# Performance work log

Hardware: AMD Instinct MI355X
Metric: run time of the kernel (lower is better)

Reference implementation:

```python
import jax, jax.numpy as jnp
import numpy as np

K_NEIGHBORS = 16  # n_sample

# Each Conv1x1+BatchNorm (eval mode) stage is an exact per-channel affine map,
# so it is represented by a single fused (W, b) pair: y = W @ x + b.

def affine(W, b, x):
    # W: [Cout, Cin]; x: [B, Cin, N] or [B, Cin, N, K]
    if x.ndim == 3:
        return jnp.einsum('oc,bcn->bon', W, x) + b[None, :, None]
    return jnp.einsum('oc,bcnk->bonk', W, x) + b[None, :, None, None]

def knn_idx(p, k):
    # p: [B, N, 3] -> idx of k nearest neighbors (incl. self): [B, N, k]
    sq = jnp.sum(p * p, axis=-1)  # [B, N]
    d2 = sq[:, :, None] + sq[:, None, :] - 2.0 * jnp.einsum('bnc,bmc->bnm', p, p)
    _, idx = jax.lax.top_k(-d2, k)
    return idx

def group(feat, idx):
    # feat: [B, C, N], idx: [B, N, K] -> grouped[b,c,n,k] = feat[b,c,idx[b,n,k]]
    return jax.vmap(lambda f, i: f[:, i])(feat, idx)


def setup_inputs() -> dict:
    key = jax.random.key(0)
    B, C, N = 4, 128, 4096
    ks = jax.random.split(key, 22)
    def w(k, o, i):
        return (jax.random.normal(k, (o, i), jnp.float32) / np.sqrt(i)).astype(jnp.float32)
    def bv(k, o):
        return (jax.random.normal(k, (o,), jnp.float32) * 0.01).astype(jnp.float32)
    inp = {
        'input_p': jax.random.normal(ks[0], (B, 3, N), jnp.float32),
        'input_x': jax.random.normal(ks[1], (B, C, N), jnp.float32),
        'top_W': w(ks[2], C, C),   'top_b': bv(ks[3], C),
        'down_W': w(ks[4], C, C),  'down_b': bv(ks[5], C),
        'phi_W': w(ks[6], C, C),   'phi_b': bv(ks[7], C),
        'psi_W': w(ks[8], C, C),   'psi_b': bv(ks[9], C),
        'alpha_W': w(ks[10], C, C), 'alpha_b': bv(ks[11], C),
        'g1_W': w(ks[12], C, C),   'g1_b': bv(ks[13], C),
        'g2_W': w(ks[14], C, C),   'g2_b': bv(ks[15], C),
        'd1_W': w(ks[16], C, 3),   'd1_b': bv(ks[17], C),
        'd2_W': w(ks[18], C, C),   'd2_b': bv(ks[19], C),
        'a': 0, 'b': 0,
    }
    return inp


def reference(input_p, input_x, top_W, top_b, down_W, down_b, phi_W, phi_b,
              psi_W, psi_b, alpha_W, alpha_b, g1_W, g1_b, g2_W, g2_b,
              d1_W, d1_b, d2_W, d2_b, a, b):
    res = input_x
    p = jnp.transpose(input_p, (0, 2, 1))          # [B, N, 3]
    idx = knn_idx(p, K_NEIGHBORS)                  # [B, N, K]
    grouped_p = group(input_p, idx)                # [B, 3, N, K]
    x = affine(top_W, top_b, input_x)              # linear_top
    phi = affine(phi_W, phi_b, x)[:, :, :, None]   # [B, C, N, 1] (broadcast over K)
    psi = group(affine(psi_W, psi_b, x), idx)      # [B, C, N, K]
    alp = group(affine(alpha_W, alpha_b, x), idx)  # [B, C, N, K]
    rel = input_p[:, :, :, None] - grouped_p       # relative xyz [B, 3, N, K]
    pos = affine(d2_W, d2_b, jax.nn.relu(affine(d1_W, d1_b, rel)))   # delta MLP
    attn = affine(g2_W, g2_b, jax.nn.relu(affine(g1_W, g1_b, phi - psi + pos)))  # gamma MLP
    y = (jax.nn.softmax(attn, axis=-1) * (alp + pos)).sum(axis=-1)   # [B, C, N]
    y = affine(down_W, down_b, y)                  # linear_down
    return y + res
```

## Files before the change

### kernel.cpp

```cpp
#include <hip/hip_runtime.h>
#include <hip/hip_bf16.h>

#define BB 4
#define CC 128
#define NN 4096
#define KK 16
#define FLT_BIG 3.402823466e+38f

typedef __attribute__((ext_vector_type(8))) short short8v;
typedef __attribute__((ext_vector_type(4))) short short4v;
typedef __attribute__((ext_vector_type(4))) float f32x4;

__device__ __forceinline__ unsigned short f2b(float x) {
  union { float f; unsigned u; } v; v.f = x;
  unsigned r = v.u + 0x7fffu + ((v.u >> 16) & 1u);
  return (unsigned short)(r >> 16);
}
__device__ __forceinline__ float b2f(unsigned short h) {
  union { float f; unsigned u; } v; v.u = ((unsigned)h) << 16; return v.f;
}

__device__ __forceinline__ float dist4(const float4 q, const float4 c) {
  float t = __fmaf_rn(q.x, c.x, __fmaf_rn(q.y, c.y, __fmul_rn(q.z, c.z)));
  return __fmaf_rn(-2.f, t, q.w + c.w);
}

__global__ __launch_bounds__(256) void prep_kernel(const float* __restrict__ p,
                                                   float4* __restrict__ pkg) {
  int i = blockIdx.x * 256 + threadIdx.x;
  int b = i >> 12, m = i & (NN - 1);
  const float* pb = p + (size_t)b * 3 * NN;
  float x = pb[m], y = pb[NN + m], z = pb[2 * NN + m];
  pkg[i] = make_float4(x, y, z, __fmaf_rn(x, x, __fmaf_rn(y, y, __fmul_rn(z, z))));
}

__global__ __launch_bounds__(256) void wprep_kernel(
    const float* __restrict__ d2W, const float* __restrict__ g1W,
    const float* __restrict__ g2W, const float* __restrict__ topW,
    const float* __restrict__ phiW, const float* __restrict__ psiW,
    const float* __restrict__ alpW, const float* __restrict__ dnW,
    unsigned short* __restrict__ wpk) {
  int t = blockIdx.x * 256 + threadIdx.x;
  int mat = t >> 11, r = t & 2047;
  int ct = r >> 8, ks = (r >> 6) & 3, lane = r & 63;
  const float* W;
  switch (mat) {
    case 0: W = d2W; break;  case 1: W = g1W; break;
    case 2: W = g2W; break;  case 3: W = topW; break;
    case 4: W = phiW; break; case 5: W = psiW; break;
    case 6: W = alpW; break; default: W = dnW; break;
  }
  int row = ct * 16 + (lane & 15);
  int k0 = ks * 32 + (lane >> 4) * 8;
  const float* src = &W[row * 128 + k0];
  unsigned short* dh = &wpk[((size_t)(((mat * 2 + 0) * 8 + ct) * 4 + ks) * 64 + lane) * 8];
  unsigned short* dl = &wpk[((size_t)(((mat * 2 + 1) * 8 + ct) * 4 + ks) * 64 + lane) * 8];
#pragma unroll
  for (int e = 0; e < 8; ++e) {
    float v = src[e];
    unsigned short h = f2b(v);
    dh[e] = h;
    dl[e] = f2b(v - b2f(h));
  }
}

__global__ __launch_bounds__(256) void xpose_kernel(const float* __restrict__ x,
                                                    unsigned short* __restrict__ xh,
                                                    unsigned short* __restrict__ xl) {
  __shared__ float t[64][65];
  const int b = blockIdx.z, c0 = blockIdx.y * 64, n0 = blockIdx.x * 64;
  const int tn = threadIdx.x & 63, tq = threadIdx.x >> 6;
  const float* xb = x + ((size_t)b * CC + c0) * NN + n0;
#pragma unroll
  for (int i = 0; i < 16; ++i) {
    int c = tq * 16 + i;
    t[c][tn] = xb[(size_t)c * NN + tn];
  }
  __syncthreads();
#pragma unroll
  for (int i = 0; i < 16; ++i) {
    int nl = tq * 16 + i;
    float v = t[tn][nl];
    unsigned short h = f2b(v);
    size_t o = ((size_t)b * NN + n0 + nl) * CC + c0 + tn;
    xh[o] = h;
    xl[o] = f2b(v - b2f(h));
  }
}

__global__ __launch_bounds__(512, 2) void knn_kernel(const float4* __restrict__ pkg,
                                                     int* __restrict__ outidx)
{
  __shared__ float BD[8][64][17];
  __shared__ float TS[64];
  __shared__ int   CNT[64];
  __shared__ float COLd[64][20];
  __shared__ int   COLi[64][20];
  const int b = blockIdx.y;
  const int tid = threadIdx.x;
  const int lane = tid & 63;
  const int w = tid >> 6;
  const int n = blockIdx.x * 64 + lane;
  const float4* PB = pkg + (size_t)b * NN;
  const float4 qc = PB[n];
  if (tid < 64) CNT[tid] = 0;

  float bd[16];
#pragma unroll
  for (int t = 0; t < 16; ++t) bd[t] = FLT_BIG;
  const int m0 = w * 512;
#pragma unroll 4
  for (int m = m0; m < m0 + 512; ++m) {
    float4 c = PB[m];
    float d = dist4(qc, c);
#pragma unroll
    for (int t = 15; t >= 1; --t) bd[t] = __builtin_amdgcn_fmed3f(bd[t - 1], d, bd[t]);
    bd[0] = fminf(bd[0], d);
  }
#pragma unroll
  for (int t = 0; t < 16; ++t) BD[w][lane][t] = bd[t];
  __syncthreads();

  if (tid < 64) {
    const int q = tid;
    int h0 = 0, h1 = 0, h2 = 0, h3 = 0, h4 = 0, h5 = 0, h6 = 0, h7 = 0;
    float mv = FLT_BIG;
#pragma unroll 1
    for (int r = 0; r < 16; ++r) {
      float v0 = BD[0][q][h0], v1 = BD[1][q][h1], v2 = BD[2][q][h2], v3 = BD[3][q][h3];
      float v4 = BD[4][q][h4], v5 = BD[5][q][h5], v6 = BD[6][q][h6], v7 = BD[7][q][h7];
      mv = v0; int mw = 0;
      if (v1 < mv) { mv = v1; mw = 1; }
      if (v2 < mv) { mv = v2; mw = 2; }
      if (v3 < mv) { mv = v3; mw = 3; }
      if (v4 < mv) { mv = v4; mw = 4; }
      if (v5 < mv) { mv = v5; mw = 5; }
      if (v6 < mv) { mv = v6; mw = 6; }
      if (v7 < mv) { mv = v7; mw = 7; }
      h0 += (mw == 0); h1 += (mw == 1); h2 += (mw == 2); h3 += (mw == 3);
      h4 += (mw == 4); h5 += (mw == 5); h6 += (mw == 6); h7 += (mw == 7);
    }
    TS[q] = mv;
  }
  __syncthreads();

  {
    const float thr = TS[lane];
#pragma unroll 4
    for (int m = m0; m < m0 + 512; ++m) {
      float4 c = PB[m];
      float d = dist4(qc, c);
      if (d <= thr) {
        int pos = atomicAdd(&CNT[lane], 1);
        if (pos < 20) { COLd[lane][pos] = d; COLi[lane][pos] = m; }
      }
    }
  }
  __syncthreads();

  if (tid < 64) {
    const int q = tid;
    int c = CNT[q]; if (c > 20) c = 20;
    int* op = outidx + ((size_t)b * NN + blockIdx.x * 64 + q) * KK;
    if (c == KK) {
#pragma unroll
      for (int o = 0; o < KK; ++o) op[o] = COLi[q][o];
    } else {
      const float T = TS[q];
      int less = 0;
      for (int s = 0; s < c; ++s) less += (COLd[q][s] < T);
      int need = KK - less;
      int o = 0;
      for (int s = 0; s < c; ++s)
        if (COLd[q][s] < T) op[o++] = COLi[q][s];
      for (int s = 0; s < c; ++s) {
        if (COLd[q][s] == T) {
          int idx = COLi[q][s];
          int rank = 0;
          for (int s2 = 0; s2 < c; ++s2)
            rank += (COLd[q][s2] == T && COLi[q][s2] < idx);
          if (rank < need) op[o++] = idx;
        }
      }
    }
  }
}

__global__ __launch_bounds__(256) void topgemm_kernel(
    const unsigned short* __restrict__ xh, const unsigned short* __restrict__ xl,
    const unsigned short* __restrict__ wpk, const float* __restrict__ bias,
    unsigned short* __restrict__ oh, unsigned short* __restrict__ ol)
{
  const int b = blockIdx.y, n0 = blockIdx.x * 32;
  const int tid = threadIdx.x, l = tid & 63, w = tid >> 6;
  const int lr = l & 15, lh = l >> 4;
  const int nt = w & 1, cq = w >> 1;
  const int nrow = n0 + nt * 16 + lr;
  const unsigned short* xhp = xh + ((size_t)b * NN + nrow) * CC;
  const unsigned short* xlp = xl + ((size_t)b * NN + nrow) * CC;
  short8v Ah[4], Al[4];
#pragma unroll
  for (int ks = 0; ks < 4; ++ks) {
    Ah[ks] = *(const short8v*)&xhp[ks * 32 + lh * 8];
    Al[ks] = *(const short8v*)&xlp[ks * 32 + lh * 8];
  }
  const int nD = n0 + nt * 16 + lh * 4;
#pragma unroll
  for (int cc = 0; cc < 4; ++cc) {
    const int colt = cq * 4 + cc;
    f32x4 acc = (f32x4){0.f, 0.f, 0.f, 0.f};
#pragma unroll
    for (int ks = 0; ks < 4; ++ks) {
      short8v Wh = *(const short8v*)&wpk[((size_t)(((3 * 2 + 0) * 8 + colt) * 4 + ks) * 64 + l) * 8];
      short8v Wl = *(const short8v*)&wpk[((size_t)(((3 * 2 + 1) * 8 + colt) * 4 + ks) * 64 + l) * 8];
      acc = __builtin_amdgcn_mfma_f32_16x16x32_bf16(Ah[ks], Wh, acc, 0, 0, 0);
      acc = __builtin_amdgcn_mfma_f32_16x16x32_bf16(Al[ks], Wh, acc, 0, 0, 0);
      acc = __builtin_amdgcn_mfma_f32_16x16x32_bf16(Ah[ks], Wl, acc, 0, 0, 0);
    }
    float bv = bias[colt * 16 + lr];
#pragma unroll
    for (int r = 0; r < 4; ++r) {
      float v = acc[r] + bv;
      unsigned short h = f2b(v);
      size_t o = ((size_t)b * NN + nD + r) * CC + colt * 16 + lr;
      oh[o] = h;
      ol[o] = f2b(v - b2f(h));
    }
  }
}

__global__ __launch_bounds__(256) void pqa_kernel(
    const unsigned short* __restrict__ xh, const unsigned short* __restrict__ xl,
    const unsigned short* __restrict__ wpk,
    const float* __restrict__ phib, const float* __restrict__ psib,
    const float* __restrict__ alpb,
    float* __restrict__ phit, float* __restrict__ psit, float* __restrict__ alpt)
{
  const int b = blockIdx.y, n0 = blockIdx.x * 32;
  const int tid = threadIdx.x, l = tid & 63, w = tid >> 6;
  const int lr = l & 15, lh = l >> 4;
  const int nt = w & 1, cq = w >> 1;
  const int nrow = n0 + nt * 16 + lr;
  const unsigned short* xhp = xh + ((size_t)b * NN + nrow) * CC;
  const unsigned short* xlp = xl + ((size_t)b * NN + nrow) * CC;
  short8v Ah[4], Al[4];
#pragma unroll
  for (int ks = 0; ks < 4; ++ks) {
    Ah[ks] = *(const short8v*)&xhp[ks * 32 + lh * 8];
    Al[ks] = *(const short8v*)&xlp[ks * 32 + lh * 8];
  }
  const int nD = n0 + nt * 16 + lh * 4;
#pragma unroll
  for (int m = 0; m < 3; ++m) {
    const int mat = 4 + m;
    const float* bias = (m == 0) ? phib : (m == 1) ? psib : alpb;
    float* outp = (m == 0) ? phit : (m == 1) ? psit : alpt;
#pragma unroll
    for (int cc = 0; cc < 4; ++cc) {
      const int colt = cq * 4 + cc;
      f32x4 acc = (f32x4){0.f, 0.f, 0.f, 0.f};
#pragma unroll
      for (int ks = 0; ks < 4; ++ks) {
        short8v Wh = *(const short8v*)&wpk[((size_t)(((mat * 2 + 0) * 8 + colt) * 4 + ks) * 64 + l) * 8];
        short8v Wl = *(const short8v*)&wpk[((size_t)(((mat * 2 + 1) * 8 + colt) * 4 + ks) * 64 + l) * 8];
        acc = __builtin_amdgcn_mfma_f32_16x16x32_bf16(Ah[ks], Wh, acc, 0, 0, 0);
        acc = __builtin_amdgcn_mfma_f32_16x16x32_bf16(Al[ks], Wh, acc, 0, 0, 0);
        acc = __builtin_amdgcn_mfma_f32_16x16x32_bf16(Ah[ks], Wl, acc, 0, 0, 0);
      }
      float bv = bias[colt * 16 + lr];
#pragma unroll
      for (int r = 0; r < 4; ++r)
        outp[((size_t)b * NN + nD + r) * CC + colt * 16 + lr] = acc[r] + bv;
    }
  }
}

__global__ __launch_bounds__(256) void down_kernel(
    const unsigned short* __restrict__ yh, const unsigned short* __restrict__ yl,
    const unsigned short* __restrict__ wpk,
    const float* __restrict__ bias, const float* __restrict__ res,
    float* __restrict__ out)
{
  const int b = blockIdx.y, n0 = blockIdx.x * 64;
  const int tid = threadIdx.x, l = tid & 63, w = tid >> 6;
  const int lr = l & 15, lh = l >> 4;
  short8v Ah[2][4], Al[2][4];
#pragma unroll
  for (int ct = 0; ct < 2; ++ct)
#pragma unroll
    for (int ks = 0; ks < 4; ++ks) {
      Ah[ct][ks] = *(const short8v*)&wpk[((size_t)(((7 * 2 + 0) * 8 + (2 * w + ct)) * 4 + ks) * 64 + l) * 8];
      Al[ct][ks] = *(const short8v*)&wpk[((size_t)(((7 * 2 + 1) * 8 + (2 * w + ct)) * 4 + ks) * 64 + l) * 8];
    }
  f32x4 acc[2][4];
#pragma unroll
  for (int colt = 0; colt < 4; ++colt) {
    const int n = n0 + colt * 16 + lr;
    const unsigned short* yhp = yh + ((size_t)b * NN + n) * CC;
    const unsigned short* ylp = yl + ((size_t)b * NN + n) * CC;
#pragma unroll
    for (int ct = 0; ct < 2; ++ct) acc[ct][colt] = (f32x4){0.f, 0.f, 0.f, 0.f};
#pragma unroll
    for (int ks = 0; ks < 4; ++ks) {
      short8v Bh = *(const short8v*)&yhp[ks * 32 + lh * 8];
      short8v Bl = *(const short8v*)&ylp[ks * 32 + lh * 8];
#pragma unroll
      for (int ct = 0; ct < 2; ++ct) {
        acc[ct][colt] = __builtin_amdgcn_mfma_f32_16x16x32_bf16(Ah[ct][ks], Bh, acc[ct][colt], 0, 0, 0);
        acc[ct][colt] = __builtin_amdgcn_mfma_f32_16x16x32_bf16(Ah[ct][ks], Bl, acc[ct][colt], 0, 0, 0);
        acc[ct][colt] = __builtin_amdgcn_mfma_f32_16x16x32_bf16(Al[ct][ks], Bh, acc[ct][colt], 0, 0, 0);
      }
    }
  }
#pragma unroll
  for (int ct = 0; ct < 2; ++ct) {
    const int c0 = 32 * w + ct * 16 + lh * 4;
#pragma unroll
    for (int r = 0; r < 4; ++r) {
      float bv = bias[c0 + r];
#pragma unroll
      for (int colt = 0; colt < 4; ++colt) {
        size_t o = ((size_t)b * CC + c0 + r) * NN + n0 + colt * 16 + lr;
        out[o] = acc[ct][colt][r] + bv + res[o];
      }
    }
  }
}

#define TNP 4
__global__ __launch_bounds__(256, 4) void fused_kernel(
    const float* __restrict__ p, const int* __restrict__ idxg,
    const float* __restrict__ phi_t, const float* __restrict__ psi_t,
    const float* __restrict__ alp_t, const unsigned short* __restrict__ wpk,
    const float* __restrict__ d1W, const float* __restrict__ d1b,
    const float* __restrict__ d2b, const float* __restrict__ g1b,
    const float* __restrict__ g2b,
    unsigned short* __restrict__ yh, unsigned short* __restrict__ yl)
{
  __shared__ __align__(16) unsigned short act[2][64][136];
  __shared__ int idxs[64];
  const int b = blockIdx.y;
  const int n0 = blockIdx.x * TNP;
  const int tid = threadIdx.x;
  const int l = tid & 63, w = tid >> 6;
  const int lr = l & 15, lh = l >> 4;

  if (tid < 64) idxs[tid] = idxg[((size_t)b * NN + n0 + (tid >> 4)) * KK + (tid & 15)];
  __syncthreads();

  {
    const int col = tid & 63, q = tid >> 6;
    const int pt = col >> 4;
    const int j = idxs[col];
    const float* pb = p + (size_t)b * 3 * NN;
    float r0 = pb[n0 + pt] - pb[j];
    float r1 = pb[NN + n0 + pt] - pb[NN + j];
    float r2 = pb[2 * NN + n0 + pt] - pb[2 * NN + j];
#pragma unroll
    for (int ch = 0; ch < 4; ++ch) {
      int c0 = q * 32 + ch * 8;
      short8v hv, lv;
#pragma unroll
      for (int e = 0; e < 8; ++e) {
        int c = c0 + e;
        float v = fmaxf(d1W[c * 3 + 0] * r0 + d1W[c * 3 + 1] * r1 + d1W[c * 3 + 2] * r2 + d1b[c], 0.f);
        unsigned short h = f2b(v);
        hv[e] = (short)h;
        lv[e] = (short)f2b(v - b2f(h));
      }
      *(short8v*)&act[0][col][c0] = hv;
      *(short8v*)&act[1][col][c0] = lv;
    }
  }
  __syncthreads();

  int idxv[TNP];
#pragma unroll
  for (int colt = 0; colt < TNP; ++colt) idxv[colt] = idxs[colt * 16 + lr];

  f32x4 acc[2][TNP];
  short8v Af[2][4];

#define LOADA(MAT) do {                                                                 \
  _Pragma("unroll") for (int ct = 0; ct < 2; ++ct)                                      \
    _Pragma("unroll") for (int ks = 0; ks < 4; ++ks)                                    \
      Af[ct][ks] = *(const short8v*)&wpk[((size_t)((((MAT) * 2 + 0) * 8 + (2 * w + ct)) * 4 + ks) * 64 + l) * 8]; \
  } while (0)

#define MMUL() do {                                                                     \
  _Pragma("unroll") for (int ct = 0; ct < 2; ++ct)                                      \
    _Pragma("unroll") for (int colt = 0; colt < TNP; ++colt)                            \
      acc[ct][colt] = (f32x4){0.f, 0.f, 0.f, 0.f};                                      \
  _Pragma("unroll") for (int colt = 0; colt < TNP; ++colt) {                            \
    short8v Bh[4], Bl[4];                                                               \
    _Pragma("unroll") for (int ks = 0; ks < 4; ++ks) {                                  \
      Bh[ks] = *(const short8v*)&act[0][colt * 16 + lr][ks * 32 + lh * 8];              \
      Bl[ks] = *(const short8v*)&act[1][colt * 16 + lr][ks * 32 + lh * 8];              \
    }                                                                                   \
    _Pragma("unroll") for (int ct = 0; ct < 2; ++ct)                                    \
      _Pragma("unroll") for (int ks = 0; ks < 4; ++ks) {                                \
        acc[ct][colt] = __builtin_amdgcn_mfma_f32_16x16x32_bf16(Af[ct][ks], Bh[ks],     \
                                                                acc[ct][colt], 0, 0, 0); \
        acc[ct][colt] = __builtin_amdgcn_mfma_f32_16x16x32_bf16(Af[ct][ks], Bl[ks],     \
                                                                acc[ct][colt], 0, 0, 0); \
      }                                                                                 \
  } } while (0)

  LOADA(0); MMUL();
  float pos[2][TNP][4];
#pragma unroll
  for (int ct = 0; ct < 2; ++ct) {
    f32x4 bv = *(const f32x4*)&d2b[32 * w + ct * 16 + lh * 4];
#pragma unroll
    for (int colt = 0; colt < TNP; ++colt)
#pragma unroll
      for (int r = 0; r < 4; ++r) pos[ct][colt][r] = acc[ct][colt][r] + bv[r];
  }
  __syncthreads();

#pragma unroll
  for (int colt = 0; colt < TNP; ++colt) {
    size_t prow = ((size_t)b * NN + n0 + colt) * CC;
    size_t srow = ((size_t)b * NN + idxv[colt]) * CC;
#pragma unroll
    for (int ct = 0; ct < 2; ++ct) {
      int c0 = 32 * w + ct * 16 + lh * 4;
      f32x4 ph = *(const f32x4*)&phi_t[prow + c0];
      f32x4 ps = *(const f32x4*)&psi_t[srow + c0];
      short4v hq, lq;
#pragma unroll
      for (int r = 0; r < 4; ++r) {
        float v = pos[ct][colt][r] + ph[r] - ps[r];
        unsigned short h = f2b(v);
        hq[r] = (short)h;
        lq[r] = (short)f2b(v - b2f(h));
      }
      *(short4v*)&act[0][colt * 16 + lr][c0] = hq;
      *(short4v*)&act[1][colt * 16 + lr][c0] = lq;
    }
  }
  __syncthreads();

  LOADA(1); MMUL();
  __syncthreads();
#pragma unroll
  for (int ct = 0; ct < 2; ++ct) {
    f32x4 bv = *(const f32x4*)&g1b[32 * w + ct * 16 + lh * 4];
    int c0 = 32 * w + ct * 16 + lh * 4;
#pragma unroll
    for (int colt = 0; colt < TNP; ++colt) {
      short4v hq, lq;
#pragma unroll
      for (int r = 0; r < 4; ++r) {
        float v = fmaxf(acc[ct][colt][r] + bv[r], 0.f);
        unsigned short h = f2b(v);
        hq[r] = (short)h;
        lq[r] = (short)f2b(v - b2f(h));
      }
      *(short4v*)&act[0][colt * 16 + lr][c0] = hq;
      *(short4v*)&act[1][colt * 16 + lr][c0] = lq;
    }
  }
  __syncthreads();

  LOADA(2); MMUL();
#pragma unroll
  for (int ct = 0; ct < 2; ++ct) {
    f32x4 bv = *(const f32x4*)&g2b[32 * w + ct * 16 + lh * 4];
#pragma unroll
    for (int colt = 0; colt < TNP; ++colt)
#pragma unroll
      for (int r = 0; r < 4; ++r) acc[ct][colt][r] += bv[r];
  }

#pragma unroll
  for (int ct = 0; ct < 2; ++ct)
#pragma unroll
    for (int colt = 0; colt < TNP; ++colt)
#pragma unroll
      for (int r = 0; r < 4; ++r) {
        float a = acc[ct][colt][r];
        float m = a;
        m = fmaxf(m, __shfl_xor(m, 1));
        m = fmaxf(m, __shfl_xor(m, 2));
        m = fmaxf(m, __shfl_xor(m, 4));
        m = fmaxf(m, __shfl_xor(m, 8));
        float e = __expf(a - m);
        float s = e;
        s += __shfl_xor(s, 1);
        s += __shfl_xor(s, 2);
        s += __shfl_xor(s, 4);
        s += __shfl_xor(s, 8);
        acc[ct][colt][r] = e / s;
      }

#pragma unroll
  for (int colt = 0; colt < TNP; ++colt) {
    size_t arow = ((size_t)b * NN + idxv[colt]) * CC;
#pragma unroll
    for (int ct = 0; ct < 2; ++ct) {
      int c0 = 32 * w + ct * 16 + lh * 4;
      f32x4 av = *(const f32x4*)&alp_t[arow + c0];
      f32x4 yv;
#pragma unroll
      for (int r = 0; r < 4; ++r) {
        float part = acc[ct][colt][r] * (av[r] + pos[ct][colt][r]);
        part += __shfl_xor(part, 1);
        part += __shfl_xor(part, 2);
        part += __shfl_xor(part, 4);
        part += __shfl_xor(part, 8);
        yv[r] = part;
      }
      if (lr == 0) {
        short4v hq, lq;
#pragma unroll
        for (int r = 0; r < 4; ++r) {
          unsigned short h = f2b(yv[r]);
          hq[r] = (short)h;
          lq[r] = (short)f2b(yv[r] - b2f(h));
        }
        size_t o = ((size_t)b * NN + n0 + colt) * CC + c0;
        *(short4v*)&yh[o] = hq;
        *(short4v*)&yl[o] = lq;
      }
    }
  }
#undef LOADA
#undef MMUL
}

extern "C" void kernel_launch(void* const* d_in, const int* in_sizes, int n_in,
                              void* d_out, int out_size, void* d_ws, size_t ws_size,
                              hipStream_t stream) {
  const float* input_p = (const float*)d_in[0];
  const float* input_x = (const float*)d_in[1];
  const float* top_W   = (const float*)d_in[2];  const float* top_b   = (const float*)d_in[3];
  const float* down_W  = (const float*)d_in[4];  const float* down_b  = (const float*)d_in[5];
  const float* phi_W   = (const float*)d_in[6];  const float* phi_b   = (const float*)d_in[7];
  const float* psi_W   = (const float*)d_in[8];  const float* psi_b   = (const float*)d_in[9];
  const float* alpha_W = (const float*)d_in[10]; const float* alpha_b = (const float*)d_in[11];
  const float* g1_W    = (const float*)d_in[12]; const float* g1_b    = (const float*)d_in[13];
  const float* g2_W    = (const float*)d_in[14]; const float* g2_b    = (const float*)d_in[15];
  const float* d1_W    = (const float*)d_in[16]; const float* d1_b    = (const float*)d_in[17];
  const float* d2_W    = (const float*)d_in[18]; const float* d2_b    = (const float*)d_in[19];
  float* out = (float*)d_out;

  char* ws = (char*)d_ws;
  int*            ws_idx = (int*)ws;
  unsigned short* ws_xin_h = (unsigned short*)(ws + (size_t)1  * (1 << 20));
  unsigned short* ws_xin_l = (unsigned short*)(ws + (size_t)5  * (1 << 20));
  unsigned short* ws_x_h   = (unsigned short*)(ws + (size_t)9  * (1 << 20));
  unsigned short* ws_x_l   = (unsigned short*)(ws + (size_t)13 * (1 << 20));
  float*          ws_phi   = (float*)(ws + (size_t)17 * (1 << 20));
  float*          ws_psi   = (float*)(ws + (size_t)25 * (1 << 20));
  float*          ws_alp   = (float*)(ws + (size_t)33 * (1 << 20));
  float4*         ws_pkg   = (float4*)(ws + (size_t)41 * (1 << 20));
  unsigned short* ws_wpk   = (unsigned short*)(ws + (size_t)41 * (1 << 20) + (1 << 18));
  unsigned short* ws_y_h = ws_xin_h;
  unsigned short* ws_y_l = ws_xin_l;

  prep_kernel<<<(BB * NN) / 256, 256, 0, stream>>>(input_p, ws_pkg);
  wprep_kernel<<<64, 256, 0, stream>>>(d2_W, g1_W, g2_W, top_W, phi_W, psi_W, alpha_W, down_W,
                                       ws_wpk);
  xpose_kernel<<<dim3(NN / 64, CC / 64, BB), 256, 0, stream>>>(input_x, ws_xin_h, ws_xin_l);
  knn_kernel<<<dim3(NN / 64, BB), 512, 0, stream>>>(ws_pkg, ws_idx);
  topgemm_kernel<<<dim3(NN / 32, BB), 256, 0, stream>>>(ws_xin_h, ws_xin_l, ws_wpk, top_b,
                                                        ws_x_h, ws_x_l);
  pqa_kernel<<<dim3(NN / 32, BB), 256, 0, stream>>>(ws_x_h, ws_x_l, ws_wpk,
                                                    phi_b, psi_b, alpha_b,
                                                    ws_phi, ws_psi, ws_alp);
  fused_kernel<<<dim3(NN / TNP, BB), 256, 0, stream>>>(input_p, ws_idx, ws_phi, ws_psi, ws_alp,
                                                       ws_wpk, d1_W, d1_b, d2_b, g1_b, g2_b,
                                                       ws_y_h, ws_y_l);
  down_kernel<<<dim3(NN / 64, BB), 256, 0, stream>>>(ws_y_h, ws_y_l, ws_wpk, down_b,
                                                     input_x, out);
}
```

Baseline: 394.4 us.

## Merge setup kernels, fuse top GEMM with projections, store alpha as bf16

Merges the three setup kernels (point packing, weight packing, transpose) into one launch, and fuses the top-linear GEMM with the phi/psi/alpha projections through a shared-memory tile, which removes the intermediate x_h/x_l round trip. Alpha is stored as a single bf16 value, halving its gather traffic but lowering its precision. In the fused kernel, psi and alpha gathers are prefetched early and bf16 hi/lo splitting uses packed conversion intrinsics. The y output is staged in LDS for coalesced 16-byte stores, at the cost of extra barriers.

```diff
diff --git a/kernel.cpp b/kernel.cpp
--- a/kernel.cpp
+++ b/kernel.cpp
@@ -19,72 +19,84 @@
 __device__ __forceinline__ float b2f(unsigned short h) {
   union { float f; unsigned u; } v; v.u = ((unsigned)h) << 16; return v.f;
 }
+__device__ __forceinline__ unsigned pkrn(float a, float b) {
+  __hip_bfloat162 t = __float22bfloat162_rn(make_float2(a, b));
+  union { __hip_bfloat162 h; unsigned u; } c; c.h = t; return c.u;
+}
+__device__ __forceinline__ void split2(float a, float b, unsigned& h, unsigned& l) {
+  h = pkrn(a, b);
+  union { unsigned u; float f; } lo, hi2;
+  lo.u = h << 16;
+  hi2.u = h & 0xffff0000u;
+  l = pkrn(a - lo.f, b - hi2.f);
+}
 
 __device__ __forceinline__ float dist4(const float4 q, const float4 c) {
   float t = __fmaf_rn(q.x, c.x, __fmaf_rn(q.y, c.y, __fmul_rn(q.z, c.z)));
   return __fmaf_rn(-2.f, t, q.w + c.w);
 }
 
-__global__ __launch_bounds__(256) void prep_kernel(const float* __restrict__ p,
-                                                   float4* __restrict__ pkg) {
-  int i = blockIdx.x * 256 + threadIdx.x;
-  int b = i >> 12, m = i & (NN - 1);
-  const float* pb = p + (size_t)b * 3 * NN;
-  float x = pb[m], y = pb[NN + m], z = pb[2 * NN + m];
-  pkg[i] = make_float4(x, y, z, __fmaf_rn(x, x, __fmaf_rn(y, y, __fmul_rn(z, z))));
-}
-
-__global__ __launch_bounds__(256) void wprep_kernel(
+__global__ __launch_bounds__(256) void setup_kernel(
+    const float* __restrict__ p, const float* __restrict__ x,
     const float* __restrict__ d2W, const float* __restrict__ g1W,
     const float* __restrict__ g2W, const float* __restrict__ topW,
     const float* __restrict__ phiW, const float* __restrict__ psiW,
     const float* __restrict__ alpW, const float* __restrict__ dnW,
-    unsigned short* __restrict__ wpk) {
-  int t = blockIdx.x * 256 + threadIdx.x;
-  int mat = t >> 11, r = t & 2047;
-  int ct = r >> 8, ks = (r >> 6) & 3, lane = r & 63;
-  const float* W;
-  switch (mat) {
-    case 0: W = d2W; break;  case 1: W = g1W; break;
-    case 2: W = g2W; break;  case 3: W = topW; break;
-    case 4: W = phiW; break; case 5: W = psiW; break;
-    case 6: W = alpW; break; default: W = dnW; break;
-  }
-  int row = ct * 16 + (lane & 15);
-  int k0 = ks * 32 + (lane >> 4) * 8;
-  const float* src = &W[row * 128 + k0];
-  unsigned short* dh = &wpk[((size_t)(((mat * 2 + 0) * 8 + ct) * 4 + ks) * 64 + lane) * 8];
-  unsigned short* dl = &wpk[((size_t)(((mat * 2 + 1) * 8 + ct) * 4 + ks) * 64 + lane) * 8];
-#pragma unroll
-  for (int e = 0; e < 8; ++e) {
-    float v = src[e];
-    unsigned short h = f2b(v);
-    dh[e] = h;
-    dl[e] = f2b(v - b2f(h));
-  }
-}
-
-__global__ __launch_bounds__(256) void xpose_kernel(const float* __restrict__ x,
-                                                    unsigned short* __restrict__ xh,
-                                                    unsigned short* __restrict__ xl) {
+    float4* __restrict__ pkg, unsigned short* __restrict__ wpk,
+    unsigned short* __restrict__ xh, unsigned short* __restrict__ xl)
+{
   __shared__ float t[64][65];
-  const int b = blockIdx.z, c0 = blockIdx.y * 64, n0 = blockIdx.x * 64;
-  const int tn = threadIdx.x & 63, tq = threadIdx.x >> 6;
-  const float* xb = x + ((size_t)b * CC + c0) * NN + n0;
-#pragma unroll
-  for (int i = 0; i < 16; ++i) {
-    int c = tq * 16 + i;
-    t[c][tn] = xb[(size_t)c * NN + tn];
-  }
-  __syncthreads();
-#pragma unroll
-  for (int i = 0; i < 16; ++i) {
-    int nl = tq * 16 + i;
-    float v = t[tn][nl];
-    unsigned short h = f2b(v);
-    size_t o = ((size_t)b * NN + n0 + nl) * CC + c0 + tn;
-    xh[o] = h;
-    xl[o] = f2b(v - b2f(h));
+  const int bid = blockIdx.x, tid = threadIdx.x;
+  if (bid < 64) {
+    int i = bid * 256 + tid;
+    int b = i >> 12, m = i & (NN - 1);
+    const float* pb = p + (size_t)b * 3 * NN;
+    float xx = pb[m], yy = pb[NN + m], zz = pb[2 * NN + m];
+    pkg[i] = make_float4(xx, yy, zz, __fmaf_rn(xx, xx, __fmaf_rn(yy, yy, __fmul_rn(zz, zz))));
+  } else if (bid < 128) {
+    int tt = (bid - 64) * 256 + tid;
+    int mat = tt >> 11, r = tt & 2047;
+    int ct = r >> 8, ks = (r >> 6) & 3, lane = r & 63;
+    const float* W;
+    switch (mat) {
+      case 0: W = d2W; break;  case 1: W = g1W; break;
+      case 2: W = g2W; break;  case 3: W = topW; break;
+      case 4: W = phiW; break; case 5: W = psiW; break;
+      case 6: W = alpW; break; default: W = dnW; break;
+    }
+    int row = ct * 16 + (lane & 15);
+    int k0 = ks * 32 + (lane >> 4) * 8;
+    const float* src = &W[row * 128 + k0];
+    unsigned short* dh = &wpk[((size_t)(((mat * 2 + 0) * 8 + ct) * 4 + ks) * 64 + lane) * 8];
+    unsigned short* dl = &wpk[((size_t)(((mat * 2 + 1) * 8 + ct) * 4 + ks) * 64 + lane) * 8];
+#pragma unroll
+    for (int e = 0; e < 8; ++e) {
+      float v = src[e];
+      unsigned short h = f2b(v);
+      dh[e] = h;
+      dl[e] = f2b(v - b2f(h));
+    }
+  } else {
+    int bid2 = bid - 128;
+    int nb = bid2 & 63, cb = (bid2 >> 6) & 1, b = bid2 >> 7;
+    const int c0 = cb * 64, n0 = nb * 64;
+    const int tn = tid & 63, tq = tid >> 6;
+    const float* xb = x + ((size_t)b * CC + c0) * NN + n0;
+#pragma unroll
+    for (int i = 0; i < 16; ++i) {
+      int c = tq * 16 + i;
+      t[c][tn] = xb[(size_t)c * NN + tn];
+    }
+    __syncthreads();
+#pragma unroll
+    for (int i = 0; i < 16; ++i) {
+      int nl = tq * 16 + i;
+      float v = t[tn][nl];
+      unsigned short h = f2b(v);
+      size_t o = ((size_t)b * NN + n0 + nl) * CC + c0 + tn;
+      xh[o] = h;
+      xl[o] = f2b(v - b2f(h));
+    }
   }
 }
 
@@ -186,75 +198,68 @@
   }
 }
 
-__global__ __launch_bounds__(256) void topgemm_kernel(
+__global__ __launch_bounds__(256) void feat_kernel(
     const unsigned short* __restrict__ xh, const unsigned short* __restrict__ xl,
-    const unsigned short* __restrict__ wpk, const float* __restrict__ bias,
-    unsigned short* __restrict__ oh, unsigned short* __restrict__ ol)
+    const unsigned short* __restrict__ wpk,
+    const float* __restrict__ topb, const float* __restrict__ phib,
+    const float* __restrict__ psib, const float* __restrict__ alpb,
+    float* __restrict__ phit, float* __restrict__ psit,
+    unsigned short* __restrict__ alpt)
 {
+  __shared__ float xtile[32][129];
   const int b = blockIdx.y, n0 = blockIdx.x * 32;
   const int tid = threadIdx.x, l = tid & 63, w = tid >> 6;
   const int lr = l & 15, lh = l >> 4;
   const int nt = w & 1, cq = w >> 1;
-  const int nrow = n0 + nt * 16 + lr;
-  const unsigned short* xhp = xh + ((size_t)b * NN + nrow) * CC;
-  const unsigned short* xlp = xl + ((size_t)b * NN + nrow) * CC;
+  {
+    const int nrow = n0 + nt * 16 + lr;
+    const unsigned short* xhp = xh + ((size_t)b * NN + nrow) * CC;
+    const unsigned short* xlp = xl + ((size_t)b * NN + nrow) * CC;
+    short8v Ah[4], Al[4];
+#pragma unroll
+    for (int ks = 0; ks < 4; ++ks) {
+      Ah[ks] = *(const short8v*)&xhp[ks * 32 + lh * 8];
+      Al[ks] = *(const short8v*)&xlp[ks * 32 + lh * 8];
+    }
+    const int nDl = nt * 16 + lh * 4;
+#pragma unroll
+    for (int cc = 0; cc < 4; ++cc) {
+      const int colt = cq * 4 + cc;
+      f32x4 acc = (f32x4){0.f, 0.f, 0.f, 0.f};
+#pragma unroll
+      for (int ks = 0; ks < 4; ++ks) {
+        short8v Wh = *(const short8v*)&wpk[((size_t)(((3 * 2 + 0) * 8 + colt) * 4 + ks) * 64 + l) * 8];
+        short8v Wl = *(const short8v*)&wpk[((size_t)(((3 * 2 + 1) * 8 + colt) * 4 + ks) * 64 + l) * 8];
+        acc = __builtin_amdgcn_mfma_f32_16x16x32_bf16(Ah[ks], Wh, acc, 0, 0, 0);
+        acc = __builtin_amdgcn_mfma_f32_16x16x32_bf16(Al[ks], Wh, acc, 0, 0, 0);
+        acc = __builtin_amdgcn_mfma_f32_16x16x32_bf16(Ah[ks], Wl, acc, 0, 0, 0);
+      }
+      float bv = topb[colt * 16 + lr];
+#pragma unroll
+      for (int r = 0; r < 4; ++r) xtile[nDl + r][colt * 16 + lr] = acc[r] + bv;
+    }
+  }
+  __syncthreads();
   short8v Ah[4], Al[4];
-#pragma unroll
-  for (int ks = 0; ks < 4; ++ks) {
-    Ah[ks] = *(const short8v*)&xhp[ks * 32 + lh * 8];
-    Al[ks] = *(const short8v*)&xlp[ks * 32 + lh * 8];
-  }
-  const int nD = n0 + nt * 16 + lh * 4;
-#pragma unroll
-  for (int cc = 0; cc < 4; ++cc) {
-    const int colt = cq * 4 + cc;
-    f32x4 acc = (f32x4){0.f, 0.f, 0.f, 0.f};
+  {
+    const int rl = nt * 16 + lr;
 #pragma unroll
     for (int ks = 0; ks < 4; ++ks) {
-      short8v Wh = *(const short8v*)&wpk[((size_t)(((3 * 2 + 0) * 8 + colt) * 4 + ks) * 64 + l) * 8];
-      short8v Wl = *(const short8v*)&wpk[((size_t)(((3 * 2 + 1) * 8 + colt) * 4 + ks) * 64 + l) * 8];
-      acc = __builtin_amdgcn_mfma_f32_16x16x32_bf16(Ah[ks], Wh, acc, 0, 0, 0);
-      acc = __builtin_amdgcn_mfma_f32_16x16x32_bf16(Al[ks], Wh, acc, 0, 0, 0);
-      acc = __builtin_amdgcn_mfma_f32_16x16x32_bf16(Ah[ks], Wl, acc, 0, 0, 0);
-    }
-    float bv = bias[colt * 16 + lr];
-#pragma unroll
-    for (int r = 0; r < 4; ++r) {
-      float v = acc[r] + bv;
-      unsigned short h = f2b(v);
-      size_t o = ((size_t)b * NN + nD + r) * CC + colt * 16 + lr;
-      oh[o] = h;
-      ol[o] = f2b(v - b2f(h));
-    }
-  }
-}
-
-__global__ __launch_bounds__(256) void pqa_kernel(
-    const unsigned short* __restrict__ xh, const unsigned short* __restrict__ xl,
-    const unsigned short* __restrict__ wpk,
-    const float* __restrict__ phib, const float* __restrict__ psib,
-    const float* __restrict__ alpb,
-    float* __restrict__ phit, float* __restrict__ psit, float* __restrict__ alpt)
-{
-  const int b = blockIdx.y, n0 = blockIdx.x * 32;
-  const int tid = threadIdx.x, l = tid & 63, w = tid >> 6;
-  const int lr = l & 15, lh = l >> 4;
-  const int nt = w & 1, cq = w >> 1;
-  const int nrow = n0 + nt * 16 + lr;
-  const unsigned short* xhp = xh + ((size_t)b * NN + nrow) * CC;
-  const unsigned short* xlp = xl + ((size_t)b * NN + nrow) * CC;
-  short8v Ah[4], Al[4];
-#pragma unroll
-  for (int ks = 0; ks < 4; ++ks) {
-    Ah[ks] = *(const short8v*)&xhp[ks * 32 + lh * 8];
-    Al[ks] = *(const short8v*)&xlp[ks * 32 + lh * 8];
+      union { short8v s; unsigned u[4]; } H, L;
+#pragma unroll
+      for (int i = 0; i < 4; ++i) {
+        float a = xtile[rl][ks * 32 + lh * 8 + 2 * i];
+        float bb = xtile[rl][ks * 32 + lh * 8 + 2 * i + 1];
+        split2(a, bb, H.u[i], L.u[i]);
+      }
+      Ah[ks] = H.s; Al[ks] = L.s;
+    }
   }
   const int nD = n0 + nt * 16 + lh * 4;
 #pragma unroll
   for (int m = 0; m < 3; ++m) {
     const int mat = 4 + m;
     const float* bias = (m == 0) ? phib : (m == 1) ? psib : alpb;
-    float* outp = (m == 0) ? phit : (m == 1) ? psit : alpt;
 #pragma unroll
     for (int cc = 0; cc < 4; ++cc) {
       const int colt = cq * 4 + cc;
@@ -268,9 +273,16 @@
         acc = __builtin_amdgcn_mfma_f32_16x16x32_bf16(Ah[ks], Wl, acc, 0, 0, 0);
       }
       float bv = bias[colt * 16 + lr];
-#pragma unroll
-      for (int r = 0; r < 4; ++r)
-        outp[((size_t)b * NN + nD + r) * CC + colt * 16 + lr] = acc[r] + bv;
+      if (m == 2) {
+#pragma unroll
+        for (int r = 0; r < 4; ++r)
+          alpt[((size_t)b * NN + nD + r) * CC + colt * 16 + lr] = f2b(acc[r] + bv);
+      } else {
+        float* outp = (m == 0) ? phit : psit;
+#pragma unroll
+        for (int r = 0; r < 4; ++r)
+          outp[((size_t)b * NN + nD + r) * CC + colt * 16 + lr] = acc[r] + bv;
+      }
     }
   }
 }
@@ -331,7 +343,7 @@
 __global__ __launch_bounds__(256, 4) void fused_kernel(
     const float* __restrict__ p, const int* __restrict__ idxg,
     const float* __restrict__ phi_t, const float* __restrict__ psi_t,
-    const float* __restrict__ alp_t, const unsigned short* __restrict__ wpk,
+    const unsigned short* __restrict__ alp_b, const unsigned short* __restrict__ wpk,
     const float* __restrict__ d1W, const float* __restrict__ d1b,
     const float* __restrict__ d2b, const float* __restrict__ g1b,
     const float* __restrict__ g2b,
@@ -359,17 +371,17 @@
 #pragma unroll
     for (int ch = 0; ch < 4; ++ch) {
       int c0 = q * 32 + ch * 8;
-      short8v hv, lv;
+      float v[8];
 #pragma unroll
       for (int e = 0; e < 8; ++e) {
         int c = c0 + e;
-        float v = fmaxf(d1W[c * 3 + 0] * r0 + d1W[c * 3 + 1] * r1 + d1W[c * 3 + 2] * r2 + d1b[c], 0.f);
-        unsigned short h = f2b(v);
-        hv[e] = (short)h;
-        lv[e] = (short)f2b(v - b2f(h));
-      }
-      *(short8v*)&act[0][col][c0] = hv;
-      *(short8v*)&act[1][col][c0] = lv;
+        v[e] = fmaxf(d1W[c * 3 + 0] * r0 + d1W[c * 3 + 1] * r1 + d1W[c * 3 + 2] * r2 + d1b[c], 0.f);
+      }
+      uint4 H, L;
+      split2(v[0], v[1], H.x, L.x); split2(v[2], v[3], H.y, L.y);
+      split2(v[4], v[5], H.z, L.z); split2(v[6], v[7], H.w, L.w);
+      *(uint4*)&act[0][col][c0] = H;
+      *(uint4*)&act[1][col][c0] = L;
     }
   }
   __syncthreads();
@@ -406,6 +418,15 @@
       }                                                                                 \
   } } while (0)
 
+  f32x4 psiv[2][TNP];
+#pragma unroll
+  for (int colt = 0; colt < TNP; ++colt) {
+    size_t srow = ((size_t)b * NN + idxv[colt]) * CC;
+#pragma unroll
+    for (int ct = 0; ct < 2; ++ct)
+      psiv[ct][colt] = *(const f32x4*)&psi_t[srow + 32 * w + ct * 16 + lh * 4];
+  }
+
   LOADA(0); MMUL();
   float pos[2][TNP][4];
 #pragma unroll
@@ -421,25 +442,29 @@
 #pragma unroll
   for (int colt = 0; colt < TNP; ++colt) {
     size_t prow = ((size_t)b * NN + n0 + colt) * CC;
-    size_t srow = ((size_t)b * NN + idxv[colt]) * CC;
 #pragma unroll
     for (int ct = 0; ct < 2; ++ct) {
       int c0 = 32 * w + ct * 16 + lh * 4;
       f32x4 ph = *(const f32x4*)&phi_t[prow + c0];
-      f32x4 ps = *(const f32x4*)&psi_t[srow + c0];
-      short4v hq, lq;
-#pragma unroll
-      for (int r = 0; r < 4; ++r) {
-        float v = pos[ct][colt][r] + ph[r] - ps[r];
-        unsigned short h = f2b(v);
-        hq[r] = (short)h;
-        lq[r] = (short)f2b(v - b2f(h));
-      }
-      *(short4v*)&act[0][colt * 16 + lr][c0] = hq;
-      *(short4v*)&act[1][colt * 16 + lr][c0] = lq;
-    }
-  }
-  __syncthreads();
+      float v[4];
+#pragma unroll
+      for (int r = 0; r < 4; ++r) v[r] = pos[ct][colt][r] + ph[r] - psiv[ct][colt][r];
+      uint2 H, L;
+      split2(v[0], v[1], H.x, L.x); split2(v[2], v[3], H.y, L.y);
+      *(uint2*)&act[0][colt * 16 + lr][c0] = H;
+      *(uint2*)&act[1][colt * 16 + lr][c0] = L;
+    }
+  }
+  __syncthreads();
+
+  uint2 ualp[2][TNP];
+#pragma unroll
+  for (int colt = 0; colt < TNP; ++colt) {
+    size_t arow = ((size_t)b * NN + idxv[colt]) * CC;
+#pragma unroll
+    for (int ct = 0; ct < 2; ++ct)
+      ualp[ct][colt] = *(const uint2*)&alp_b[arow + 32 * w + ct * 16 + lh * 4];
+  }
 
   LOADA(1); MMUL();
   __syncthreads();
@@ -449,16 +474,13 @@
     int c0 = 32 * w + ct * 16 + lh * 4;
 #pragma unroll
     for (int colt = 0; colt < TNP; ++colt) {
-      short4v hq, lq;
-#pragma unroll
-      for (int r = 0; r < 4; ++r) {
-        float v = fmaxf(acc[ct][colt][r] + bv[r], 0.f);
-        unsigned short h = f2b(v);
-        hq[r] = (short)h;
-        lq[r] = (short)f2b(v - b2f(h));
-      }
-      *(short4v*)&act[0][colt * 16 + lr][c0] = hq;
-      *(short4v*)&act[1][colt * 16 + lr][c0] = lq;
+      float v[4];
+#pragma unroll
+      for (int r = 0; r < 4; ++r) v[r] = fmaxf(acc[ct][colt][r] + bv[r], 0.f);
+      uint2 H, L;
+      split2(v[0], v[1], H.x, L.x); split2(v[2], v[3], H.y, L.y);
+      *(uint2*)&act[0][colt * 16 + lr][c0] = H;
+      *(uint2*)&act[1][colt * 16 + lr][c0] = L;
     }
   }
   __syncthreads();
@@ -494,14 +516,20 @@
         acc[ct][colt][r] = e / s;
       }
 
+  __syncthreads();
+  unsigned short* yst = &act[0][0][0];
+
 #pragma unroll
   for (int colt = 0; colt < TNP; ++colt) {
-    size_t arow = ((size_t)b * NN + idxv[colt]) * CC;
 #pragma unroll
     for (int ct = 0; ct < 2; ++ct) {
       int c0 = 32 * w + ct * 16 + lh * 4;
-      f32x4 av = *(const f32x4*)&alp_t[arow + c0];
-      f32x4 yv;
+      uint2 ua = ualp[ct][colt];
+      union { unsigned u; float f; } a0, a1, a2, a3;
+      a0.u = ua.x << 16; a1.u = ua.x & 0xffff0000u;
+      a2.u = ua.y << 16; a3.u = ua.y & 0xffff0000u;
+      float av[4] = {a0.f, a1.f, a2.f, a3.f};
+      float yv[4];
 #pragma unroll
       for (int r = 0; r < 4; ++r) {
         float part = acc[ct][colt][r] * (av[r] + pos[ct][colt][r]);
@@ -512,18 +540,19 @@
         yv[r] = part;
       }
       if (lr == 0) {
-        short4v hq, lq;
-#pragma unroll
-        for (int r = 0; r < 4; ++r) {
-          unsigned short h = f2b(yv[r]);
-          hq[r] = (short)h;
-          lq[r] = (short)f2b(yv[r] - b2f(h));
-        }
-        size_t o = ((size_t)b * NN + n0 + colt) * CC + c0;
-        *(short4v*)&yh[o] = hq;
-        *(short4v*)&yl[o] = lq;
-      }
-    }
+        uint2 H, L;
+        split2(yv[0], yv[1], H.x, L.x); split2(yv[2], yv[3], H.y, L.y);
+        *(uint2*)&yst[(size_t)colt * 128 + c0] = H;
+        *(uint2*)&yst[(size_t)(4 + colt) * 128 + c0] = L;
+      }
+    }
+  }
+  __syncthreads();
+  if (tid < 128) {
+    int plane = tid >> 6, row = (tid >> 4) & 3, chunk = tid & 15;
+    uint4 v4 = *(const uint4*)&yst[(size_t)(plane * 4 + row) * 128 + chunk * 8];
+    unsigned short* dst = (plane ? yl : yh) + ((size_t)b * NN + n0 + row) * CC + chunk * 8;
+    *(uint4*)dst = v4;
   }
 #undef LOADA
 #undef MMUL
@@ -546,29 +575,24 @@
   float* out = (float*)d_out;
 
   char* ws = (char*)d_ws;
-  int*            ws_idx = (int*)ws;
+  int*            ws_idx   = (int*)ws;
   unsigned short* ws_xin_h = (unsigned short*)(ws + (size_t)1  * (1 << 20));
   unsigned short* ws_xin_l = (unsigned short*)(ws + (size_t)5  * (1 << 20));
-  unsigned short* ws_x_h   = (unsigned short*)(ws + (size_t)9  * (1 << 20));
-  unsigned short* ws_x_l   = (unsigned short*)(ws + (size_t)13 * (1 << 20));
-  float*          ws_phi   = (float*)(ws + (size_t)17 * (1 << 20));
-  float*          ws_psi   = (float*)(ws + (size_t)25 * (1 << 20));
-  float*          ws_alp   = (float*)(ws + (size_t)33 * (1 << 20));
-  float4*         ws_pkg   = (float4*)(ws + (size_t)41 * (1 << 20));
-  unsigned short* ws_wpk   = (unsigned short*)(ws + (size_t)41 * (1 << 20) + (1 << 18));
+  float*          ws_phi   = (float*)(ws + (size_t)9  * (1 << 20));
+  float*          ws_psi   = (float*)(ws + (size_t)17 * (1 << 20));
+  unsigned short* ws_alp   = (unsigned short*)(ws + (size_t)25 * (1 << 20));
+  float4*         ws_pkg   = (float4*)(ws + (size_t)29 * (1 << 20));
+  unsigned short* ws_wpk   = (unsigned short*)(ws + (size_t)29 * (1 << 20) + (1 << 18));
   unsigned short* ws_y_h = ws_xin_h;
   unsigned short* ws_y_l = ws_xin_l;
 
-  prep_kernel<<<(BB * NN) / 256, 256, 0, stream>>>(input_p, ws_pkg);
-  wprep_kernel<<<64, 256, 0, stream>>>(d2_W, g1_W, g2_W, top_W, phi_W, psi_W, alpha_W, down_W,
-                                       ws_wpk);
-  xpose_kernel<<<dim3(NN / 64, CC / 64, BB), 256, 0, stream>>>(input_x, ws_xin_h, ws_xin_l);
+  setup_kernel<<<640, 256, 0, stream>>>(input_p, input_x, d2_W, g1_W, g2_W, top_W,
+                                        phi_W, psi_W, alpha_W, down_W,
+                                        ws_pkg, ws_wpk, ws_xin_h, ws_xin_l);
   knn_kernel<<<dim3(NN / 64, BB), 512, 0, stream>>>(ws_pkg, ws_idx);
-  topgemm_kernel<<<dim3(NN / 32, BB), 256, 0, stream>>>(ws_xin_h, ws_xin_l, ws_wpk, top_b,
-                                                        ws_x_h, ws_x_l);
-  pqa_kernel<<<dim3(NN / 32, BB), 256, 0, stream>>>(ws_x_h, ws_x_l, ws_wpk,
-                                                    phi_b, psi_b, alpha_b,
-                                                    ws_phi, ws_psi, ws_alp);
+  feat_kernel<<<dim3(NN / 32, BB), 256, 0, stream>>>(ws_xin_h, ws_xin_l, ws_wpk,
+                                                     top_b, phi_b, psi_b, alpha_b,
+                                                     ws_phi, ws_psi, ws_alp);
   fused_kernel<<<dim3(NN / TNP, BB), 256, 0, stream>>>(input_p, ws_idx, ws_phi, ws_psi, ws_alp,
                                                        ws_wpk, d1_W, d1_b, d2_b, g1_b, g2_b,
                                                        ws_y_h, ws_y_l);
```

After: 391.6 us. No clear change (-0.7%).
